# Optimization experiments

Measured on AMD Instinct MI355X. Metric: run time of the kernel, lower is better.

Reference implementation:

```python
import jax, jax.numpy as jnp
import numpy as np

HEAD_SIZE = 128
BLOCK_SIZE = 2048


def setup_inputs() -> dict:
    key = jax.random.key(0)
    kx, kk, kq, kv = jax.random.split(key, 4)
    B, T, C = 8, 2048, HEAD_SIZE
    s = 1.0 / np.sqrt(C)
    x = jax.random.normal(kx, (B, T, C), dtype=jnp.float32)
    Wk = jax.random.normal(kk, (C, C), dtype=jnp.float32) * s
    Wq = jax.random.normal(kq, (C, C), dtype=jnp.float32) * s
    Wv = jax.random.normal(kv, (C, C), dtype=jnp.float32) * s
    return {"x": x, "Wk": Wk, "Wq": Wq, "Wv": Wv}


def reference(x, Wk, Wq, Wv):
    B, T, C = x.shape
    # nn.Linear(C, C, bias=False): y = x @ W.T
    k = jnp.einsum('btc,dc->btd', x, Wk)
    q = jnp.einsum('btc,dc->btd', x, Wq)
    v = jnp.einsum('btc,dc->btd', x, Wv)
    scores = jnp.einsum('btd,bsd->bts', q, k) * (C ** -0.5)  # [B,T,T]
    causal = jnp.tril(jnp.ones((T, T), dtype=bool))
    scores = jnp.where(causal, scores, -jnp.inf)
    weights = jax.nn.softmax(scores, axis=-1)
    return jnp.einsum('bts,bsd->btd', weights, v)
```

## Files before the change

### kernel.cpp

```cpp
#include <hip/hip_runtime.h>

#define T_SEQ 2048
#define C_DIM 128
#define S_QK 0.08838834764831845f

typedef __attribute__((ext_vector_type(8))) short bf16x8;
typedef __attribute__((ext_vector_type(4))) short bf16x4;
typedef __attribute__((ext_vector_type(4))) float f32x4;
typedef __attribute__((ext_vector_type(2))) unsigned int u32x2;

#define OPART_OFF 12582912UL
#define ML_OFF    43778048UL

#define GLOAD_LDS16(gp, lp)                                          \
    __builtin_amdgcn_global_load_lds(                                \
        (const __attribute__((address_space(1))) void*)(gp),         \
        (__attribute__((address_space(3))) void*)(lp), 16, 0, 0)

__device__ __forceinline__ unsigned short f2bf(float f) {
    union { float f; unsigned int u; } v; v.f = f;
    unsigned int r = v.u + 0x7FFFu + ((v.u >> 16) & 1u);
    return (unsigned short)(r >> 16);
}

__device__ __forceinline__ f32x4 mfma16(bf16x4 a, bf16x4 b, f32x4 c) {
#if __has_builtin(__builtin_amdgcn_mfma_f32_16x16x16_bf16_1k)
    return __builtin_amdgcn_mfma_f32_16x16x16_bf16_1k(a, b, c, 0, 0, 0);
#elif __has_builtin(__builtin_amdgcn_mfma_f32_16x16x16_bf16)
    return __builtin_amdgcn_mfma_f32_16x16x16_bf16(a, b, c, 0, 0, 0);
#else
    f32x4 d = c;
    asm("v_mfma_f32_16x16x16_bf16 %0, %1, %2, %0" : "+v"(d) : "v"(a), "v"(b));
    return d;
#endif
}

__device__ __forceinline__ int base5(int qt) {
    int g = qt / 5 + 1;
    return 5 * g * (g - 1) / 2 + (qt - 5 * (g - 1)) * g;
}

__global__ __launch_bounds__(256) void proj_kernel(
    const float* __restrict__ x,
    const float* __restrict__ Wk, const float* __restrict__ Wq,
    const float* __restrict__ Wv,
    unsigned short* __restrict__ qo, unsigned short* __restrict__ ko,
    unsigned short* __restrict__ vto)
{
    const int rt = blockIdx.x;
    const int z  = blockIdx.y;
    const int tid  = threadIdx.x;
    const int lane = tid & 63;
    const int w    = tid >> 6;
    const int n16  = lane & 15;
    const int quad = lane >> 4;

    __shared__ __align__(16) unsigned short Wl[128 * 136];
    __shared__ __align__(16) unsigned short Xl[9216];

    const float* Wsrc = (z == 0 ? Wq : z == 1 ? Wk : Wv);
    const float wscale = (z == 0) ? S_QK : 1.0f;
    #pragma unroll
    for (int i = 0; i < 16; ++i) {
        int e = (tid + i * 256) * 4;
        int r = e >> 7, c = e & 127;
        float4 v = *reinterpret_cast<const float4*>(Wsrc + e);
        float ax = v.x * wscale, ay = v.y * wscale;
        float az = v.z * wscale, aw = v.w * wscale;
        unsigned lo, hi;
        asm("v_cvt_pk_bf16_f32 %0, %1, %2" : "=v"(lo) : "v"(ax), "v"(ay));
        asm("v_cvt_pk_bf16_f32 %0, %1, %2" : "=v"(hi) : "v"(az), "v"(aw));
        uint2 o2; o2.x = lo; o2.y = hi;
        *reinterpret_cast<uint2*>(&Wl[r * 136 + c]) = o2;
    }
    const float* xrow = x + (size_t)rt * 64 * C_DIM;
    #pragma unroll
    for (int i = 0; i < 8; ++i) {
        int e = (tid + i * 256) * 4;
        int r = e >> 7, c = e & 127;
        float4 v = *reinterpret_cast<const float4*>(xrow + e);
        unsigned lo, hi;
        asm("v_cvt_pk_bf16_f32 %0, %1, %2" : "=v"(lo) : "v"(v.x), "v"(v.y));
        asm("v_cvt_pk_bf16_f32 %0, %1, %2" : "=v"(hi) : "v"(v.z), "v"(v.w));
        uint2 o2; o2.x = lo; o2.y = hi;
        *reinterpret_cast<uint2*>(&Xl[r * 136 + c]) = o2;
    }
    __syncthreads();

    const int arow = w * 16 + n16;
    bf16x8 afr[4];
    #pragma unroll
    for (int kk = 0; kk < 4; ++kk)
        afr[kk] = *reinterpret_cast<const bf16x8*>(&Xl[arow * 136 + kk * 32 + quad * 8]);

    f32x4 acc[8];
    #pragma unroll
    for (int nt = 0; nt < 8; ++nt) acc[nt] = (f32x4){0.f, 0.f, 0.f, 0.f};
    #pragma unroll
    for (int kk = 0; kk < 4; ++kk)
        #pragma unroll
        for (int nt = 0; nt < 8; ++nt) {
            bf16x8 bfr = *reinterpret_cast<const bf16x8*>(
                &Wl[(nt * 16 + n16) * 136 + kk * 32 + quad * 8]);
            acc[nt] = __builtin_amdgcn_mfma_f32_16x16x32_bf16(afr[kk], bfr, acc[nt], 0, 0, 0);
        }

    const int trow_base = w * 16 + quad * 4;
    __syncthreads();
    if (z < 2) {
        #pragma unroll
        for (int nt = 0; nt < 8; ++nt)
            #pragma unroll
            for (int r = 0; r < 4; ++r)
                Xl[(trow_base + r) * 136 + nt * 16 + n16] = f2bf(acc[nt][r]);
        __syncthreads();
        unsigned short* dst = (z == 0 ? qo : ko) + (size_t)rt * 64 * C_DIM;
        #pragma unroll
        for (int i = 0; i < 4; ++i) {
            int e = (tid + i * 256) * 8;
            int r = e >> 7, c = e & 127;
            *reinterpret_cast<uint4*>(dst + e) =
                *reinterpret_cast<const uint4*>(&Xl[r * 136 + c]);
        }
    } else {
        const int b  = rt >> 5;
        const int qt = rt & 31;
        #pragma unroll
        for (int nt = 0; nt < 8; ++nt)
            #pragma unroll
            for (int r = 0; r < 4; ++r)
                Xl[(nt * 16 + n16) * 72 + trow_base + r] = f2bf(acc[nt][r]);
        __syncthreads();
        unsigned short* dst = vto + (size_t)b * C_DIM * T_SEQ + (size_t)qt * 64;
        #pragma unroll
        for (int i = 0; i < 4; ++i) {
            int e = tid + i * 256;
            int d = e >> 3, cv = (e & 7) * 8;
            *reinterpret_cast<uint4*>(dst + (size_t)d * T_SEQ + cv) =
                *reinterpret_cast<const uint4*>(&Xl[d * 72 + cv]);
        }
    }
}

__device__ __forceinline__ void stage_tile32(
    const char* ksb, const char* vsb,
    unsigned short* klbuf, unsigned short* vlbuf, int tid, int w)
{
    #pragma unroll
    for (int it = 0; it < 2; ++it) {
        const int L = it * 256 + tid;
        const int r = L >> 4, c = L & 15;
        GLOAD_LDS16(ksb + r * 256 + ((c ^ (r & 7)) << 4),
                    klbuf + (size_t)(it * 256 + w * 64) * 8);
    }
    #pragma unroll
    for (int it = 0; it < 2; ++it) {
        const int L = it * 256 + tid;
        const int r = L >> 2, c = L & 3;
        GLOAD_LDS16(vsb + (size_t)r * (T_SEQ * 2) +
                        ((c ^ (r & 3) ^ ((r >> 2) & 3)) << 4),
                    vlbuf + (size_t)(it * 256 + w * 64) * 8);
    }
}

__global__ __launch_bounds__(256, 4) void attn_kernel(
    const unsigned short* __restrict__ qb,
    const unsigned short* __restrict__ kb,
    const unsigned short* __restrict__ vtb,
    float* __restrict__ opart, float2* __restrict__ mlbuf,
    float* __restrict__ out)
{
    const int lin = blockIdx.x;
    const int b   = lin & 7;
    const int s   = lin >> 3;
    int g = 1, gbase = 0;
    while (s - gbase >= 5 * g) { gbase += 5 * g; ++g; }
    const int qt    = 5 * (g - 1) + (s - gbase) / g;
    const int chunk = (s - gbase) % g;
    const int nch   = g;

    const int tid  = threadIdx.x;
    const int lane = tid & 63;
    const int w    = tid >> 6;
    const int n16  = lane & 15;
    const int quad = lane >> 4;

    __shared__ __align__(16) unsigned short Kl[2][32 * 128];
    __shared__ __align__(16) unsigned short Vl[2][128 * 32];

    const size_t bT = (size_t)b * T_SEQ;
    const int qbase = qt * 64 + w * 16;
    const int ulim  = 4 * qt + w;

    const int st0 = chunk * 10;
    const int st1 = min(st0 + 10, 2 * qt + 2);

    const char* kbase = (const char*)(kb + bT * C_DIM);
    const char* vbase = (const char*)(vtb + (size_t)b * C_DIM * T_SEQ);

    stage_tile32(kbase + (size_t)st0 * 8192, vbase + (size_t)st0 * 64,
                 Kl[0], Vl[0], tid, w);

    bf16x8 qfr[4];
    #pragma unroll
    for (int kk = 0; kk < 4; ++kk)
        qfr[kk] = *reinterpret_cast<const bf16x8*>(
            qb + (bT + qbase + n16) * C_DIM + kk * 32 + quad * 8);

    f32x4 o[8];
    #pragma unroll
    for (int ct = 0; ct < 8; ++ct) o[ct] = (f32x4){0.f, 0.f, 0.f, 0.f};
    float m_ = -INFINITY, l_ = 0.f;

    const int kx  = n16 & 7;
    const int sig = (n16 & 3) ^ ((n16 >> 2) & 3);
    const int vof0 = n16 * 32 + (((quad >> 1) ^ sig) << 3) + (quad & 1) * 4;
    const int vof1 = n16 * 32 + ((((quad >> 1) + 2) ^ sig) << 3) + (quad & 1) * 4;

    int cur = 0;
    for (int st = st0; st < st1; ++st, cur ^= 1) {
        if (st + 1 < st1) {
            stage_tile32(kbase + (size_t)(st + 1) * 8192,
                         vbase + (size_t)(st + 1) * 64,
                         Kl[cur ^ 1], Vl[cur ^ 1], tid, w);
            asm volatile("s_waitcnt vmcnt(4)" ::: "memory");
        } else {
            asm volatile("s_waitcnt vmcnt(0)" ::: "memory");
        }
        __builtin_amdgcn_s_barrier();

        const unsigned short* klc = Kl[cur];
        const unsigned short* vlc = Vl[cur];

        #pragma unroll
        for (int sub = 0; sub < 2; ++sub) {
            const int u = st * 2 + sub;
            if (u <= ulim) {
                f32x4 s4 = (f32x4){0.f, 0.f, 0.f, 0.f};
                const unsigned short* krow = klc + (sub * 16 + n16) * 128;
                __builtin_amdgcn_s_setprio(1);
                #pragma unroll
                for (int kk = 0; kk < 4; ++kk) {
                    bf16x8 kfr = *reinterpret_cast<const bf16x8*>(
                        krow + (((kk * 4 + quad) ^ kx) << 3));
                    s4 = __builtin_amdgcn_mfma_f32_16x16x32_bf16(kfr, qfr[kk], s4, 0, 0, 0);
                }
                __builtin_amdgcn_s_setprio(0);

                if (u == ulim) {
                    #pragma unroll
                    for (int r = 0; r < 4; ++r) {
                        int sabs = u * 16 + quad * 4 + r;
                        if (sabs > qbase + n16) s4[r] = -1e30f;
                    }
                }

                float pmax = fmaxf(fmaxf(s4[0], s4[1]), fmaxf(s4[2], s4[3]));
                pmax = fmaxf(pmax, __shfl_xor(pmax, 16));
                pmax = fmaxf(pmax, __shfl_xor(pmax, 32));
                if (pmax > m_ + 8.f) {
                    float alpha = __expf(m_ - pmax);
                    l_ *= alpha;
                    #pragma unroll
                    for (int ct = 0; ct < 8; ++ct) {
                        o[ct][0] *= alpha; o[ct][1] *= alpha;
                        o[ct][2] *= alpha; o[ct][3] *= alpha;
                    }
                    m_ = pmax;
                }
                float p0 = __expf(s4[0] - m_), p1 = __expf(s4[1] - m_);
                float p2 = __expf(s4[2] - m_), p3 = __expf(s4[3] - m_);
                float ts = (p0 + p1) + (p2 + p3);
                ts += __shfl_xor(ts, 16);
                ts += __shfl_xor(ts, 32);
                l_ += ts;

                unsigned plo, phi;
                asm("v_cvt_pk_bf16_f32 %0, %1, %2" : "=v"(plo) : "v"(p0), "v"(p1));
                asm("v_cvt_pk_bf16_f32 %0, %1, %2" : "=v"(phi) : "v"(p2), "v"(p3));
                u32x2 pp; pp.x = plo; pp.y = phi;
                bf16x4 pv = __builtin_bit_cast(bf16x4, pp);

                const int vof = sub ? vof1 : vof0;
                __builtin_amdgcn_s_setprio(1);
                #pragma unroll
                for (int ct = 0; ct < 8; ++ct) {
                    bf16x4 vfr = *reinterpret_cast<const bf16x4*>(vlc + ct * 512 + vof);
                    o[ct] = mfma16(vfr, pv, o[ct]);
                }
                __builtin_amdgcn_s_setprio(0);
            }
        }

        asm volatile("s_waitcnt lgkmcnt(0)" ::: "memory");
        __builtin_amdgcn_s_barrier();
    }

    if (nch == 1) {
        float* outp = out + (bT + qbase + n16) * C_DIM;
        const float inv = 1.0f / l_;
        #pragma unroll
        for (int ct = 0; ct < 8; ++ct) {
            float4 r4;
            r4.x = o[ct][0] * inv; r4.y = o[ct][1] * inv;
            r4.z = o[ct][2] * inv; r4.w = o[ct][3] * inv;
            *reinterpret_cast<float4*>(outp + ct * 16 + quad * 4) = r4;
        }
        return;
    }

    const int slot = b * 119 + s;
    float* op = opart + (size_t)slot * 8192 + (size_t)(w * 16 + n16) * 128;
    #pragma unroll
    for (int ct = 0; ct < 8; ++ct) {
        float4 r4;
        r4.x = o[ct][0]; r4.y = o[ct][1];
        r4.z = o[ct][2]; r4.w = o[ct][3];
        *reinterpret_cast<float4*>(op + ct * 16 + quad * 4) = r4;
    }
    if (quad == 0)
        mlbuf[(size_t)slot * 64 + w * 16 + n16] = make_float2(m_, l_);
}

__global__ __launch_bounds__(256) void merge_kernel(
    const float* __restrict__ opart, const float2* __restrict__ mlbuf,
    float* __restrict__ out)
{
    const int qt = 5 + blockIdx.x;
    const int b  = blockIdx.y;
    const int nch  = qt / 5 + 1;
    const int base = b * 119 + base5(qt);
    const int row = threadIdx.x >> 2;
    const int c0  = (threadIdx.x & 3) * 32;

    float mi[7], li[7], wgt[7];
    float M = -INFINITY;
    #pragma unroll
    for (int i = 0; i < 7; ++i) {
        if (i < nch) {
            float2 t = mlbuf[(size_t)(base + i) * 64 + row];
            mi[i] = t.x; li[i] = t.y;
            M = fmaxf(M, t.x);
        } else { mi[i] = -INFINITY; li[i] = 0.f; }
    }
    float L = 0.f;
    #pragma unroll
    for (int i = 0; i < 7; ++i) {
        wgt[i] = (i < nch) ? __expf(mi[i] - M) : 0.f;
        L += li[i] * wgt[i];
    }
    const float inv = 1.0f / L;

    float* orow = out + ((size_t)(b * T_SEQ + qt * 64 + row)) * C_DIM;
    #pragma unroll
    for (int j = 0; j < 8; ++j) {
        int col = c0 + j * 4;
        float ax = 0.f, ay = 0.f, az = 0.f, aw = 0.f;
        #pragma unroll
        for (int i = 0; i < 7; ++i) {
            if (i < nch) {
                float4 p = *reinterpret_cast<const float4*>(
                    opart + (size_t)(base + i) * 8192 + row * 128 + col);
                ax += wgt[i] * p.x; ay += wgt[i] * p.y;
                az += wgt[i] * p.z; aw += wgt[i] * p.w;
            }
        }
        float4 r4; r4.x = ax * inv; r4.y = ay * inv; r4.z = az * inv; r4.w = aw * inv;
        *reinterpret_cast<float4*>(orow + col) = r4;
    }
}

extern "C" void kernel_launch(void* const* d_in, const int* in_sizes, int n_in,
                              void* d_out, int out_size, void* d_ws, size_t ws_size,
                              hipStream_t stream) {
    const float* x  = (const float*)d_in[0];
    const float* Wk = (const float*)d_in[1];
    const float* Wq = (const float*)d_in[2];
    const float* Wv = (const float*)d_in[3];

    unsigned short* qw  = (unsigned short*)d_ws;
    unsigned short* kw  = qw + 2097152;
    unsigned short* vw  = kw + 2097152;
    float*          opart = (float*)((char*)d_ws + OPART_OFF);
    float2*         mlb   = (float2*)((char*)d_ws + ML_OFF);

    proj_kernel<<<dim3(256, 3), 256, 0, stream>>>(x, Wk, Wq, Wv, qw, kw, vw);
    attn_kernel<<<dim3(952), 256, 0, stream>>>(qw, kw, vw, opart, mlb, (float*)d_out);
    merge_kernel<<<dim3(27, 8), 256, 0, stream>>>(opart, mlb, (float*)d_out);
}
```

Measured before the change: 123.1 us.

## Rework attention so each wave owns 32 query rows and reads K/V directly

Replaces the LDS-staged, block-shared K/V double buffer with per-wave direct global loads of K and V fragments. Each wave now handles two 16-row query sub-tiles that reuse the same K/V fragments. The split-KV schedule is redone with 32-row query tiles, chunks of 16 key tiles, and a new partial/merge layout. This removes LDS staging and block barriers at the cost of more global/L2 traffic per wave, higher register pressure (occupancy hint lowered to 3), and a different load balance across waves.

Measured after the change: 159.6 us. 1.3x slower.

```diff
diff --git a/kernel.cpp b/kernel.cpp
--- a/kernel.cpp
+++ b/kernel.cpp
@@ -10,12 +10,7 @@
 typedef __attribute__((ext_vector_type(2))) unsigned int u32x2;
 
 #define OPART_OFF 12582912UL
-#define ML_OFF    43778048UL
-
-#define GLOAD_LDS16(gp, lp)                                          \
-    __builtin_amdgcn_global_load_lds(                                \
-        (const __attribute__((address_space(1))) void*)(gp),         \
-        (__attribute__((address_space(3))) void*)(lp), 16, 0, 0)
+#define ML_OFF    50331648UL
 
 __device__ __forceinline__ unsigned short f2bf(float f) {
     union { float f; unsigned int u; } v; v.f = f;
@@ -33,11 +28,6 @@
     asm("v_mfma_f32_16x16x16_bf16 %0, %1, %2, %0" : "+v"(d) : "v"(a), "v"(b));
     return d;
 #endif
-}
-
-__device__ __forceinline__ int base5(int qt) {
-    int g = qt / 5 + 1;
-    return 5 * g * (g - 1) / 2 + (qt - 5 * (g - 1)) * g;
 }
 
 __global__ __launch_bounds__(256) void proj_kernel(
@@ -142,225 +132,230 @@
     }
 }
 
-__device__ __forceinline__ void stage_tile32(
-    const char* ksb, const char* vsb,
-    unsigned short* klbuf, unsigned short* vlbuf, int tid, int w)
-{
-    #pragma unroll
-    for (int it = 0; it < 2; ++it) {
-        const int L = it * 256 + tid;
-        const int r = L >> 4, c = L & 15;
-        GLOAD_LDS16(ksb + r * 256 + ((c ^ (r & 7)) << 4),
-                    klbuf + (size_t)(it * 256 + w * 64) * 8);
-    }
-    #pragma unroll
-    for (int it = 0; it < 2; ++it) {
-        const int L = it * 256 + tid;
-        const int r = L >> 2, c = L & 3;
-        GLOAD_LDS16(vsb + (size_t)r * (T_SEQ * 2) +
-                        ((c ^ (r & 3) ^ ((r >> 2) & 3)) << 4),
-                    vlbuf + (size_t)(it * 256 + w * 64) * 8);
-    }
-}
-
-__global__ __launch_bounds__(256, 4) void attn_kernel(
+__global__ __launch_bounds__(256, 3) void attn_kernel(
     const unsigned short* __restrict__ qb,
     const unsigned short* __restrict__ kb,
     const unsigned short* __restrict__ vtb,
     float* __restrict__ opart, float2* __restrict__ mlbuf,
     float* __restrict__ out)
 {
-    const int lin = blockIdx.x;
-    const int b   = lin & 7;
-    const int s   = lin >> 3;
-    int g = 1, gbase = 0;
-    while (s - gbase >= 5 * g) { gbase += 5 * g; ++g; }
-    const int qt    = 5 * (g - 1) + (s - gbase) / g;
-    const int chunk = (s - gbase) % g;
-    const int nch   = g;
-
-    const int tid  = threadIdx.x;
-    const int lane = tid & 63;
-    const int w    = tid >> 6;
+    const int b    = blockIdx.x & 7;
+    const int w    = threadIdx.x >> 6;
+    const int si   = (blockIdx.x >> 3) * 4 + w;
+    const int lane = threadIdx.x & 63;
     const int n16  = lane & 15;
     const int quad = lane >> 4;
 
-    __shared__ __align__(16) unsigned short Kl[2][32 * 128];
-    __shared__ __align__(16) unsigned short Vl[2][128 * 32];
+    int g = 0;
+    while (si >= 4 * (g + 1) * (g + 2)) ++g;
+    const int rem   = si - 4 * g * (g + 1);
+    const int qi    = 8 * g + rem / (g + 1);
+    const int chunk = rem % (g + 1);
+    const int nch   = g + 1;
 
     const size_t bT = (size_t)b * T_SEQ;
-    const int qbase = qt * 64 + w * 16;
-    const int ulim  = 4 * qt + w;
-
-    const int st0 = chunk * 10;
-    const int st1 = min(st0 + 10, 2 * qt + 2);
-
-    const char* kbase = (const char*)(kb + bT * C_DIM);
-    const char* vbase = (const char*)(vtb + (size_t)b * C_DIM * T_SEQ);
-
-    stage_tile32(kbase + (size_t)st0 * 8192, vbase + (size_t)st0 * 64,
-                 Kl[0], Vl[0], tid, w);
-
-    bf16x8 qfr[4];
-    #pragma unroll
-    for (int kk = 0; kk < 4; ++kk)
-        qfr[kk] = *reinterpret_cast<const bf16x8*>(
-            qb + (bT + qbase + n16) * C_DIM + kk * 32 + quad * 8);
-
-    f32x4 o[8];
-    #pragma unroll
-    for (int ct = 0; ct < 8; ++ct) o[ct] = (f32x4){0.f, 0.f, 0.f, 0.f};
-    float m_ = -INFINITY, l_ = 0.f;
-
-    const int kx  = n16 & 7;
-    const int sig = (n16 & 3) ^ ((n16 >> 2) & 3);
-    const int vof0 = n16 * 32 + (((quad >> 1) ^ sig) << 3) + (quad & 1) * 4;
-    const int vof1 = n16 * 32 + ((((quad >> 1) + 2) ^ sig) << 3) + (quad & 1) * 4;
-
-    int cur = 0;
-    for (int st = st0; st < st1; ++st, cur ^= 1) {
-        if (st + 1 < st1) {
-            stage_tile32(kbase + (size_t)(st + 1) * 8192,
-                         vbase + (size_t)(st + 1) * 64,
-                         Kl[cur ^ 1], Vl[cur ^ 1], tid, w);
-            asm volatile("s_waitcnt vmcnt(4)" ::: "memory");
-        } else {
-            asm volatile("s_waitcnt vmcnt(0)" ::: "memory");
-        }
-        __builtin_amdgcn_s_barrier();
-
-        const unsigned short* klc = Kl[cur];
-        const unsigned short* vlc = Vl[cur];
-
-        #pragma unroll
-        for (int sub = 0; sub < 2; ++sub) {
-            const int u = st * 2 + sub;
-            if (u <= ulim) {
-                f32x4 s4 = (f32x4){0.f, 0.f, 0.f, 0.f};
-                const unsigned short* krow = klc + (sub * 16 + n16) * 128;
-                __builtin_amdgcn_s_setprio(1);
-                #pragma unroll
-                for (int kk = 0; kk < 4; ++kk) {
-                    bf16x8 kfr = *reinterpret_cast<const bf16x8*>(
-                        krow + (((kk * 4 + quad) ^ kx) << 3));
-                    s4 = __builtin_amdgcn_mfma_f32_16x16x32_bf16(kfr, qfr[kk], s4, 0, 0, 0);
-                }
-                __builtin_amdgcn_s_setprio(0);
-
-                if (u == ulim) {
-                    #pragma unroll
-                    for (int r = 0; r < 4; ++r) {
-                        int sabs = u * 16 + quad * 4 + r;
-                        if (sabs > qbase + n16) s4[r] = -1e30f;
-                    }
-                }
-
-                float pmax = fmaxf(fmaxf(s4[0], s4[1]), fmaxf(s4[2], s4[3]));
-                pmax = fmaxf(pmax, __shfl_xor(pmax, 16));
-                pmax = fmaxf(pmax, __shfl_xor(pmax, 32));
-                if (pmax > m_ + 8.f) {
-                    float alpha = __expf(m_ - pmax);
-                    l_ *= alpha;
-                    #pragma unroll
-                    for (int ct = 0; ct < 8; ++ct) {
-                        o[ct][0] *= alpha; o[ct][1] *= alpha;
-                        o[ct][2] *= alpha; o[ct][3] *= alpha;
-                    }
-                    m_ = pmax;
-                }
-                float p0 = __expf(s4[0] - m_), p1 = __expf(s4[1] - m_);
-                float p2 = __expf(s4[2] - m_), p3 = __expf(s4[3] - m_);
-                float ts = (p0 + p1) + (p2 + p3);
-                ts += __shfl_xor(ts, 16);
-                ts += __shfl_xor(ts, 32);
-                l_ += ts;
-
-                unsigned plo, phi;
-                asm("v_cvt_pk_bf16_f32 %0, %1, %2" : "=v"(plo) : "v"(p0), "v"(p1));
-                asm("v_cvt_pk_bf16_f32 %0, %1, %2" : "=v"(phi) : "v"(p2), "v"(p3));
-                u32x2 pp; pp.x = plo; pp.y = phi;
-                bf16x4 pv = __builtin_bit_cast(bf16x4, pp);
-
-                const int vof = sub ? vof1 : vof0;
-                __builtin_amdgcn_s_setprio(1);
+    const int qA = 32 * qi + n16;
+    const int u0 = chunk * 16;
+    const int u1 = min(u0 + 16, 2 * qi + 2);
+    const int uA = 2 * qi;
+
+    const unsigned short* qp = qb + (bT + qA) * C_DIM + quad * 8;
+    bf16x8 qfrA[4], qfrB[4];
+    #pragma unroll
+    for (int kk = 0; kk < 4; ++kk) {
+        qfrA[kk] = *reinterpret_cast<const bf16x8*>(qp + kk * 32);
+        qfrB[kk] = *reinterpret_cast<const bf16x8*>(qp + 16 * C_DIM + kk * 32);
+    }
+
+    f32x4 oA[8], oB[8];
+    #pragma unroll
+    for (int ct = 0; ct < 8; ++ct) {
+        oA[ct] = (f32x4){0.f, 0.f, 0.f, 0.f};
+        oB[ct] = (f32x4){0.f, 0.f, 0.f, 0.f};
+    }
+    float mA = -INFINITY, lA = 0.f, mB = -INFINITY, lB = 0.f;
+
+    const unsigned short* kp = kb + bT * C_DIM + (size_t)u0 * 16 * C_DIM
+                               + n16 * C_DIM + quad * 8;
+    const unsigned short* vp = vtb + (size_t)b * C_DIM * T_SEQ
+                               + (size_t)n16 * T_SEQ + u0 * 16 + quad * 4;
+
+    for (int u = u0; u < u1; ++u) {
+        bf16x8 kfr0 = *reinterpret_cast<const bf16x8*>(kp);
+        bf16x8 kfr1 = *reinterpret_cast<const bf16x8*>(kp + 32);
+        bf16x8 kfr2 = *reinterpret_cast<const bf16x8*>(kp + 64);
+        bf16x8 kfr3 = *reinterpret_cast<const bf16x8*>(kp + 96);
+        bf16x4 vfr[8];
+        #pragma unroll
+        for (int ct = 0; ct < 8; ++ct)
+            vfr[ct] = *reinterpret_cast<const bf16x4*>(vp + (size_t)ct * 32768);
+
+        const bool hasA = (u <= uA);
+
+        f32x4 sB = (f32x4){0.f, 0.f, 0.f, 0.f};
+        __builtin_amdgcn_s_setprio(1);
+        sB = __builtin_amdgcn_mfma_f32_16x16x32_bf16(kfr0, qfrB[0], sB, 0, 0, 0);
+        sB = __builtin_amdgcn_mfma_f32_16x16x32_bf16(kfr1, qfrB[1], sB, 0, 0, 0);
+        sB = __builtin_amdgcn_mfma_f32_16x16x32_bf16(kfr2, qfrB[2], sB, 0, 0, 0);
+        sB = __builtin_amdgcn_mfma_f32_16x16x32_bf16(kfr3, qfrB[3], sB, 0, 0, 0);
+        f32x4 sA = (f32x4){0.f, 0.f, 0.f, 0.f};
+        if (hasA) {
+            sA = __builtin_amdgcn_mfma_f32_16x16x32_bf16(kfr0, qfrA[0], sA, 0, 0, 0);
+            sA = __builtin_amdgcn_mfma_f32_16x16x32_bf16(kfr1, qfrA[1], sA, 0, 0, 0);
+            sA = __builtin_amdgcn_mfma_f32_16x16x32_bf16(kfr2, qfrA[2], sA, 0, 0, 0);
+            sA = __builtin_amdgcn_mfma_f32_16x16x32_bf16(kfr3, qfrA[3], sA, 0, 0, 0);
+        }
+        __builtin_amdgcn_s_setprio(0);
+
+        if (u == uA) {
+            #pragma unroll
+            for (int r = 0; r < 4; ++r)
+                if (u * 16 + quad * 4 + r > qA) sA[r] = -1e30f;
+        }
+        if (u == uA + 1) {
+            #pragma unroll
+            for (int r = 0; r < 4; ++r)
+                if (u * 16 + quad * 4 + r > qA + 16) sB[r] = -1e30f;
+        }
+
+        {
+            float pmax = fmaxf(fmaxf(sB[0], sB[1]), fmaxf(sB[2], sB[3]));
+            pmax = fmaxf(pmax, __shfl_xor(pmax, 16));
+            pmax = fmaxf(pmax, __shfl_xor(pmax, 32));
+            if (pmax > mB + 8.f) {
+                float alpha = __expf(mB - pmax);
+                lB *= alpha;
                 #pragma unroll
                 for (int ct = 0; ct < 8; ++ct) {
-                    bf16x4 vfr = *reinterpret_cast<const bf16x4*>(vlc + ct * 512 + vof);
-                    o[ct] = mfma16(vfr, pv, o[ct]);
+                    oB[ct][0] *= alpha; oB[ct][1] *= alpha;
+                    oB[ct][2] *= alpha; oB[ct][3] *= alpha;
                 }
-                __builtin_amdgcn_s_setprio(0);
+                mB = pmax;
             }
-        }
-
-        asm volatile("s_waitcnt lgkmcnt(0)" ::: "memory");
-        __builtin_amdgcn_s_barrier();
-    }
+            float p0 = __expf(sB[0] - mB), p1 = __expf(sB[1] - mB);
+            float p2 = __expf(sB[2] - mB), p3 = __expf(sB[3] - mB);
+            lB += (p0 + p1) + (p2 + p3);
+            unsigned plo, phi;
+            asm("v_cvt_pk_bf16_f32 %0, %1, %2" : "=v"(plo) : "v"(p0), "v"(p1));
+            asm("v_cvt_pk_bf16_f32 %0, %1, %2" : "=v"(phi) : "v"(p2), "v"(p3));
+            u32x2 pp; pp.x = plo; pp.y = phi;
+            bf16x4 pv = __builtin_bit_cast(bf16x4, pp);
+            __builtin_amdgcn_s_setprio(1);
+            #pragma unroll
+            for (int ct = 0; ct < 8; ++ct)
+                oB[ct] = mfma16(vfr[ct], pv, oB[ct]);
+            __builtin_amdgcn_s_setprio(0);
+        }
+        if (hasA) {
+            float pmax = fmaxf(fmaxf(sA[0], sA[1]), fmaxf(sA[2], sA[3]));
+            pmax = fmaxf(pmax, __shfl_xor(pmax, 16));
+            pmax = fmaxf(pmax, __shfl_xor(pmax, 32));
+            if (pmax > mA + 8.f) {
+                float alpha = __expf(mA - pmax);
+                lA *= alpha;
+                #pragma unroll
+                for (int ct = 0; ct < 8; ++ct) {
+                    oA[ct][0] *= alpha; oA[ct][1] *= alpha;
+                    oA[ct][2] *= alpha; oA[ct][3] *= alpha;
+                }
+                mA = pmax;
+            }
+            float p0 = __expf(sA[0] - mA), p1 = __expf(sA[1] - mA);
+            float p2 = __expf(sA[2] - mA), p3 = __expf(sA[3] - mA);
+            lA += (p0 + p1) + (p2 + p3);
+            unsigned plo, phi;
+            asm("v_cvt_pk_bf16_f32 %0, %1, %2" : "=v"(plo) : "v"(p0), "v"(p1));
+            asm("v_cvt_pk_bf16_f32 %0, %1, %2" : "=v"(phi) : "v"(p2), "v"(p3));
+            u32x2 pp; pp.x = plo; pp.y = phi;
+            bf16x4 pv = __builtin_bit_cast(bf16x4, pp);
+            __builtin_amdgcn_s_setprio(1);
+            #pragma unroll
+            for (int ct = 0; ct < 8; ++ct)
+                oA[ct] = mfma16(vfr[ct], pv, oA[ct]);
+            __builtin_amdgcn_s_setprio(0);
+        }
+
+        kp += 16 * C_DIM;
+        vp += 16;
+    }
+
+    lA += __shfl_xor(lA, 16); lA += __shfl_xor(lA, 32);
+    lB += __shfl_xor(lB, 16); lB += __shfl_xor(lB, 32);
 
     if (nch == 1) {
-        float* outp = out + (bT + qbase + n16) * C_DIM;
-        const float inv = 1.0f / l_;
+        float* oa = out + (bT + qA) * C_DIM + quad * 4;
+        float* ob = oa + 16 * C_DIM;
+        const float invA = 1.0f / lA, invB = 1.0f / lB;
         #pragma unroll
         for (int ct = 0; ct < 8; ++ct) {
-            float4 r4;
-            r4.x = o[ct][0] * inv; r4.y = o[ct][1] * inv;
-            r4.z = o[ct][2] * inv; r4.w = o[ct][3] * inv;
-            *reinterpret_cast<float4*>(outp + ct * 16 + quad * 4) = r4;
+            float4 ra, rb;
+            ra.x = oA[ct][0] * invA; ra.y = oA[ct][1] * invA;
+            ra.z = oA[ct][2] * invA; ra.w = oA[ct][3] * invA;
+            rb.x = oB[ct][0] * invB; rb.y = oB[ct][1] * invB;
+            rb.z = oB[ct][2] * invB; rb.w = oB[ct][3] * invB;
+            *reinterpret_cast<float4*>(oa + ct * 16) = ra;
+            *reinterpret_cast<float4*>(ob + ct * 16) = rb;
         }
         return;
     }
 
-    const int slot = b * 119 + s;
-    float* op = opart + (size_t)slot * 8192 + (size_t)(w * 16 + n16) * 128;
+    const int slot = b * 288 + si;
+    float* op = opart + (size_t)slot * 4096 + n16 * 128 + quad * 4;
     #pragma unroll
     for (int ct = 0; ct < 8; ++ct) {
-        float4 r4;
-        r4.x = o[ct][0]; r4.y = o[ct][1];
-        r4.z = o[ct][2]; r4.w = o[ct][3];
-        *reinterpret_cast<float4*>(op + ct * 16 + quad * 4) = r4;
-    }
-    if (quad == 0)
-        mlbuf[(size_t)slot * 64 + w * 16 + n16] = make_float2(m_, l_);
+        float4 ra, rb;
+        ra.x = oA[ct][0]; ra.y = oA[ct][1]; ra.z = oA[ct][2]; ra.w = oA[ct][3];
+        rb.x = oB[ct][0]; rb.y = oB[ct][1]; rb.z = oB[ct][2]; rb.w = oB[ct][3];
+        *reinterpret_cast<float4*>(op + ct * 16) = ra;
+        *reinterpret_cast<float4*>(op + 16 * 128 + ct * 16) = rb;
+    }
+    if (quad == 0) {
+        mlbuf[(size_t)slot * 32 + n16]      = make_float2(mA, lA);
+        mlbuf[(size_t)slot * 32 + 16 + n16] = make_float2(mB, lB);
+    }
 }
 
 __global__ __launch_bounds__(256) void merge_kernel(
     const float* __restrict__ opart, const float2* __restrict__ mlbuf,
     float* __restrict__ out)
 {
-    const int qt = 5 + blockIdx.x;
+    const int qi = 8 + blockIdx.x;
     const int b  = blockIdx.y;
-    const int nch  = qt / 5 + 1;
-    const int base = b * 119 + base5(qt);
-    const int row = threadIdx.x >> 2;
-    const int c0  = (threadIdx.x & 3) * 32;
-
-    float mi[7], li[7], wgt[7];
+    const int g  = qi >> 3;
+    const int t  = qi & 7;
+    const int nch  = g + 1;
+    const int base = b * 288 + (g + 1) * (4 * g + t);
+    const int row = threadIdx.x >> 3;
+    const int c0  = (threadIdx.x & 7) * 16;
+
+    float mi[8], li[8], wgt[8];
     float M = -INFINITY;
     #pragma unroll
-    for (int i = 0; i < 7; ++i) {
+    for (int i = 0; i < 8; ++i) {
         if (i < nch) {
-            float2 t = mlbuf[(size_t)(base + i) * 64 + row];
-            mi[i] = t.x; li[i] = t.y;
-            M = fmaxf(M, t.x);
+            float2 tv = mlbuf[(size_t)(base + i) * 32 + row];
+            mi[i] = tv.x; li[i] = tv.y;
+            M = fmaxf(M, tv.x);
         } else { mi[i] = -INFINITY; li[i] = 0.f; }
     }
     float L = 0.f;
     #pragma unroll
-    for (int i = 0; i < 7; ++i) {
+    for (int i = 0; i < 8; ++i) {
         wgt[i] = (i < nch) ? __expf(mi[i] - M) : 0.f;
         L += li[i] * wgt[i];
     }
     const float inv = 1.0f / L;
 
-    float* orow = out + ((size_t)(b * T_SEQ + qt * 64 + row)) * C_DIM;
-    #pragma unroll
-    for (int j = 0; j < 8; ++j) {
+    float* orow = out + ((size_t)(b * T_SEQ + qi * 32 + row)) * C_DIM;
+    #pragma unroll
+    for (int j = 0; j < 4; ++j) {
         int col = c0 + j * 4;
         float ax = 0.f, ay = 0.f, az = 0.f, aw = 0.f;
         #pragma unroll
-        for (int i = 0; i < 7; ++i) {
+        for (int i = 0; i < 8; ++i) {
             if (i < nch) {
                 float4 p = *reinterpret_cast<const float4*>(
-                    opart + (size_t)(base + i) * 8192 + row * 128 + col);
+                    opart + (size_t)(base + i) * 4096 + row * 128 + col);
                 ax += wgt[i] * p.x; ay += wgt[i] * p.y;
                 az += wgt[i] * p.z; aw += wgt[i] * p.w;
             }
@@ -385,6 +380,6 @@
     float2*         mlb   = (float2*)((char*)d_ws + ML_OFF);
 
     proj_kernel<<<dim3(256, 3), 256, 0, stream>>>(x, Wk, Wq, Wv, qw, kw, vw);
-    attn_kernel<<<dim3(952), 256, 0, stream>>>(qw, kw, vw, opart, mlb, (float*)d_out);
-    merge_kernel<<<dim3(27, 8), 256, 0, stream>>>(opart, mlb, (float*)d_out);
-}
+    attn_kernel<<<dim3(576), 256, 0, stream>>>(qw, kw, vw, opart, mlb, (float*)d_out);
+    merge_kernel<<<dim3(56, 8), 256, 0, stream>>>(opart, mlb, (float*)d_out);
+}
```
